# Performance work log

Hardware: AMD Instinct MI355X
Metric: run time of the kernel (lower is better)

Reference implementation:

```python
import jax, jax.numpy as jnp
import numpy as np

EPS = 1e-07


def _windowed_sum(x, window):
    """Zero-padded (TF SAME, stride 1) sliding-window sum along axis 1 via cumsum.
    x: [B, S, C] -> [B, S, C]."""
    pad_left = (window - 1) // 2
    pad_right = (window - 1) - pad_left
    xp = jnp.pad(x, ((0, 0), (pad_left, pad_right), (0, 0)))  # [B, S+W-1, C]
    cs = jnp.cumsum(xp, axis=1)
    cs = jnp.concatenate([jnp.zeros_like(cs[:, :1]), cs], axis=1)  # [B, S+W, C]
    return cs[:, window:] - cs[:, :-window]  # [B, S, C]


def setup_inputs() -> dict:
    key = jax.random.key(0)
    inputs = jax.random.normal(key, (32, 8192, 128), dtype=jnp.float32)
    return {"inputs": inputs, "window_size": 24}


def reference(inputs, window_size):
    W = window_size
    B, S, C = inputs.shape
    # TF AveragePooling1D with SAME padding averages over VALID elements only
    # (padded zeros are excluded from the count).
    ones = jnp.ones((1, S, 1), dtype=inputs.dtype)
    count = _windowed_sum(ones, W)  # [1, S, 1] valid-element counts
    moving_mean = _windowed_sum(inputs, W) / count  # [B, S, C]
    sq = jnp.square(inputs - moving_mean)
    # conv1d with all-ones [W, C, C] kernel, SAME padding: every output channel
    # equals the zero-padded windowed sum of sq summed over ALL input channels.
    sq_tot = jnp.sum(sq, axis=-1, keepdims=True)  # [B, S, 1]
    moving_variance = _windowed_sum(sq_tot, W) / (W - 1)  # [B, S, 1]
    moving_std = jnp.sqrt(moving_variance)  # broadcasts over channels
    return (inputs - moving_mean) / (moving_std + EPS)
```

## Files before the change

kernel.cpp:

```cpp
#include <hip/hip_runtime.h>
#include <math.h>


constexpr int Sdim = 8192;
constexpr int Cdim = 128;
constexpr int TT   = 256;
constexpr int NTb  = Sdim / TT;
constexpr float EPSv = 1e-7f;

typedef unsigned int uintx2 __attribute__((ext_vector_type(2)));

template<bool EDGE>
__device__ __forceinline__ float2 ldg(const float* __restrict__ base, int r) {
    if (EDGE && (unsigned)r >= (unsigned)Sdim) return make_float2(0.f, 0.f);
    return *reinterpret_cast<const float2*>(base + (size_t)r * Cdim);
}

__device__ __forceinline__ void st2(float* p, float a, float b) {
    *reinterpret_cast<float2*>(p) = make_float2(a, b);
}

template<int N>
__device__ __forceinline__ float dpp_ror_add(float v) {
    int r = __builtin_amdgcn_update_dpp(0, __float_as_int(v),
                                        0x120 | N, 0xf, 0xf, true);
    return v + __int_as_float(r);
}

__device__ __forceinline__ float swap32_add(float v) {
    const unsigned u = __float_as_uint(v);
    uintx2 r = __builtin_amdgcn_permlane32_swap(u, u, false, false);
    return __uint_as_float(r.x) + __uint_as_float(r.y);
}

__device__ __forceinline__ float swap16_add(float v) {
    const unsigned u = __float_as_uint(v);
    uintx2 r = __builtin_amdgcn_permlane16_swap(u, u, false, false);
    return __uint_as_float(r.x) + __uint_as_float(r.y);
}

__device__ __forceinline__ float wave_allsum(float v) {
    v = swap32_add(v);
    v = swap16_add(v);
    v = dpp_ror_add<8>(v);
    v = dpp_ror_add<4>(v);
    v = dpp_ror_add<2>(v);
    v = dpp_ror_add<1>(v);
    return v;
}

template<bool EDGE, bool LOAD, int NJ>
__device__ __forceinline__ void chunkN(
    const float* __restrict__ base, float* __restrict__ obase,
    float2 (&Xw)[12], float2 (&Xm)[12], float2 (&Xn)[12],
    float (&Tw)[12], float (&Tr)[12], float2 (&Lb)[12],
    float2& lead, float& varsum, int cb, int t0)
{
    float2 onum[4];
    float  vs4[4];
#pragma unroll
    for (int j = 0; j < NJ; ++j) {
        const int s = cb + j;
        const float2 xold = Xw[j];
        if (LOAD) Xw[j] = ldg<EDGE>(base, s + 24);
        const float2 xmid = Xn[j];
        lead.x += xmid.x - xold.x;
        lead.y += xmid.y - xold.y;
        const float2 xcur = Xm[j];
        float invc;
        if (EDGE) {
            const int cnt = min(s + 12, Sdim - 1) - max(s - 11, 0) + 1;
            invc = __builtin_amdgcn_rcpf((float)cnt);
        } else {
            invc = 1.f / 24.f;
        }
        const float dx = xcur.x - lead.x * invc;
        const float dy = xcur.y - lead.y * invc;
        float st = dx * dx + dy * dy;
        if (EDGE && (unsigned)s >= (unsigned)Sdim) st = 0.f;
        varsum += st - Tr[j];
        Tw[j] = st;
        const float2 wq = Lb[j];
        Lb[j] = lead;
        float invq;
        if (EDGE) {
            const int q = s - 12;
            const int cq = min(q + 12, Sdim - 1) - max(q - 11, 0) + 1;
            invq = __builtin_amdgcn_rcpf((float)cq);
        } else {
            invq = 1.f / 24.f;
        }
        onum[j & 3].x = xold.x - wq.x * invq;
        onum[j & 3].y = xold.y - wq.y * invq;
        vs4[j & 3] = varsum;

        if ((j & 3) == 3) {
            const int q0 = s - 15;
            if (q0 >= t0 && q0 < t0 + TT) {
                const float r0 = wave_allsum(vs4[0]);
                const float r1 = wave_allsum(vs4[1]);
                const float r2 = wave_allsum(vs4[2]);
                const float r3 = wave_allsum(vs4[3]);
                const float i0 = __builtin_amdgcn_rcpf(
                    __builtin_amdgcn_sqrtf(fmaxf(r0, 0.f) * (1.f / 23.f)) + EPSv);
                const float i1 = __builtin_amdgcn_rcpf(
                    __builtin_amdgcn_sqrtf(fmaxf(r1, 0.f) * (1.f / 23.f)) + EPSv);
                const float i2 = __builtin_amdgcn_rcpf(
                    __builtin_amdgcn_sqrtf(fmaxf(r2, 0.f) * (1.f / 23.f)) + EPSv);
                const float i3 = __builtin_amdgcn_rcpf(
                    __builtin_amdgcn_sqrtf(fmaxf(r3, 0.f) * (1.f / 23.f)) + EPSv);
                st2(obase + (size_t)(q0    ) * Cdim, onum[0].x * i0, onum[0].y * i0);
                st2(obase + (size_t)(q0 + 1) * Cdim, onum[1].x * i1, onum[1].y * i1);
                st2(obase + (size_t)(q0 + 2) * Cdim, onum[2].x * i2, onum[2].y * i2);
                st2(obase + (size_t)(q0 + 3) * Cdim, onum[3].x * i3, onum[3].y * i3);
            }
        }
    }
}

template<bool EDGE>
__device__ __forceinline__ void run_tile(
    const float* __restrict__ base, float* __restrict__ obase, int t0)
{
    float2 X0[12], X1[12], X2[12], Lb[12];
    float  T0[12], T1[12], T2[12];
    float2 lead = make_float2(0.f, 0.f);
    float  varsum = 0.f;

#pragma unroll
    for (int j = 0; j < 12; ++j) {
        X0[j] = ldg<EDGE>(base, t0 - 24 + j);
        X1[j] = ldg<EDGE>(base, t0 - 12 + j);
        X2[j] = ldg<EDGE>(base, t0 + j);
        T0[j] = 0.f; T1[j] = 0.f; T2[j] = 0.f;
        Lb[j] = make_float2(0.f, 0.f);
        lead.x += X0[j].x + X1[j].x;
        lead.y += X0[j].y + X1[j].y;
    }

    int cb = t0 - 12;
#pragma unroll 1
    for (int k = 0; k < 7; ++k) {
        chunkN<EDGE, true, 12>(base, obase, X0, X1, X2, T0, T1, Lb, lead, varsum, cb, t0); cb += 12;
        chunkN<EDGE, true, 12>(base, obase, X1, X2, X0, T1, T2, Lb, lead, varsum, cb, t0); cb += 12;
        chunkN<EDGE, true, 12>(base, obase, X2, X0, X1, T2, T0, Lb, lead, varsum, cb, t0); cb += 12;
    }
    chunkN<EDGE, true , 12>(base, obase, X0, X1, X2, T0, T1, Lb, lead, varsum, cb, t0); cb += 12;
    chunkN<EDGE, true , 12>(base, obase, X1, X2, X0, T1, T2, Lb, lead, varsum, cb, t0); cb += 12;
    chunkN<EDGE, false,  4>(base, obase, X2, X0, X1, T2, T0, Lb, lead, varsum, cb, t0);
}

__global__ __launch_bounds__(256, 2)
void mzs_kernel(const float* __restrict__ x, float* __restrict__ y) {
    const int tid  = threadIdx.x;
    const int lane = tid & 63;
    const int wid  = blockIdx.x * 4 + (tid >> 6);
    const int b    = wid >> 5;
    const int ti   = wid & 31;
    const int t0   = ti * TT;
    const float* base  = x + (size_t)b * Sdim * Cdim + lane * 2;
    float*       obase = y + (size_t)b * Sdim * Cdim + lane * 2;
    if (ti == 0 || ti == NTb - 1) run_tile<true >(base, obase, t0);
    else                          run_tile<false>(base, obase, t0);
}

extern "C" void kernel_launch(void* const* d_in, const int* in_sizes, int n_in,
                              void* d_out, int out_size, void* d_ws, size_t ws_size,
                              hipStream_t stream) {
    const float* x = (const float*)d_in[0];
    float* y = (float*)d_out;
    mzs_kernel<<<dim3(256), dim3(256), 0, stream>>>(x, y);
}
```

Measured before the change: 53.56 us.

## Deepen register prefetch ring to four chunks and relax launch bounds

Adds a fourth 12-row register buffer so global loads are issued 36 rows ahead instead of 24, giving more latency hiding per wave. The main loop is restructured into a 12-chunk rotation over four buffers, with loads in the final two chunks gated by a runtime flag. Launch bounds are lowered to one block per SM to allow the larger register footprint. This risks lower occupancy, and the loop now processes 288 rows instead of the previous 268, so it does extra work. The EDGE handling for the extra rows has to be correct.

```diff
diff --git a/kernel.cpp b/kernel.cpp
--- a/kernel.cpp
+++ b/kernel.cpp
@@ -49,20 +49,20 @@
     return v;
 }
 
-template<bool EDGE, bool LOAD, int NJ>
-__device__ __forceinline__ void chunkN(
+template<bool EDGE>
+__device__ __forceinline__ void chunk12(
     const float* __restrict__ base, float* __restrict__ obase,
     float2 (&Xw)[12], float2 (&Xm)[12], float2 (&Xn)[12],
     float (&Tw)[12], float (&Tr)[12], float2 (&Lb)[12],
-    float2& lead, float& varsum, int cb, int t0)
+    float2& lead, float& varsum, int cb, int t0, bool doLoad)
 {
     float2 onum[4];
     float  vs4[4];
 #pragma unroll
-    for (int j = 0; j < NJ; ++j) {
+    for (int j = 0; j < 12; ++j) {
         const int s = cb + j;
         const float2 xold = Xw[j];
-        if (LOAD) Xw[j] = ldg<EDGE>(base, s + 24);
+        if (doLoad) Xw[j] = ldg<EDGE>(base, s + 36);
         const float2 xmid = Xn[j];
         lead.x += xmid.x - xold.x;
         lead.y += xmid.y - xold.y;
@@ -122,7 +122,7 @@
 __device__ __forceinline__ void run_tile(
     const float* __restrict__ base, float* __restrict__ obase, int t0)
 {
-    float2 X0[12], X1[12], X2[12], Lb[12];
+    float2 X0[12], X1[12], X2[12], X3[12], Lb[12];
     float  T0[12], T1[12], T2[12];
     float2 lead = make_float2(0.f, 0.f);
     float  varsum = 0.f;
@@ -132,6 +132,7 @@
         X0[j] = ldg<EDGE>(base, t0 - 24 + j);
         X1[j] = ldg<EDGE>(base, t0 - 12 + j);
         X2[j] = ldg<EDGE>(base, t0 + j);
+        X3[j] = ldg<EDGE>(base, t0 + 12 + j);
         T0[j] = 0.f; T1[j] = 0.f; T2[j] = 0.f;
         Lb[j] = make_float2(0.f, 0.f);
         lead.x += X0[j].x + X1[j].x;
@@ -140,17 +141,24 @@
 
     int cb = t0 - 12;
 #pragma unroll 1
-    for (int k = 0; k < 7; ++k) {
-        chunkN<EDGE, true, 12>(base, obase, X0, X1, X2, T0, T1, Lb, lead, varsum, cb, t0); cb += 12;
-        chunkN<EDGE, true, 12>(base, obase, X1, X2, X0, T1, T2, Lb, lead, varsum, cb, t0); cb += 12;
-        chunkN<EDGE, true, 12>(base, obase, X2, X0, X1, T2, T0, Lb, lead, varsum, cb, t0); cb += 12;
+    for (int r = 0; r < 2; ++r) {
+        const bool lt = (r == 0);
+        chunk12<EDGE>(base, obase, X0, X1, X2, T0, T1, Lb, lead, varsum, cb, t0, true); cb += 12;
+        chunk12<EDGE>(base, obase, X1, X2, X3, T1, T2, Lb, lead, varsum, cb, t0, true); cb += 12;
+        chunk12<EDGE>(base, obase, X2, X3, X0, T2, T0, Lb, lead, varsum, cb, t0, true); cb += 12;
+        chunk12<EDGE>(base, obase, X3, X0, X1, T0, T1, Lb, lead, varsum, cb, t0, true); cb += 12;
+        chunk12<EDGE>(base, obase, X0, X1, X2, T1, T2, Lb, lead, varsum, cb, t0, true); cb += 12;
+        chunk12<EDGE>(base, obase, X1, X2, X3, T2, T0, Lb, lead, varsum, cb, t0, true); cb += 12;
+        chunk12<EDGE>(base, obase, X2, X3, X0, T0, T1, Lb, lead, varsum, cb, t0, true); cb += 12;
+        chunk12<EDGE>(base, obase, X3, X0, X1, T1, T2, Lb, lead, varsum, cb, t0, true); cb += 12;
+        chunk12<EDGE>(base, obase, X0, X1, X2, T2, T0, Lb, lead, varsum, cb, t0, true); cb += 12;
+        chunk12<EDGE>(base, obase, X1, X2, X3, T0, T1, Lb, lead, varsum, cb, t0, true); cb += 12;
+        chunk12<EDGE>(base, obase, X2, X3, X0, T1, T2, Lb, lead, varsum, cb, t0, lt);   cb += 12;
+        chunk12<EDGE>(base, obase, X3, X0, X1, T2, T0, Lb, lead, varsum, cb, t0, lt);   cb += 12;
     }
-    chunkN<EDGE, true , 12>(base, obase, X0, X1, X2, T0, T1, Lb, lead, varsum, cb, t0); cb += 12;
-    chunkN<EDGE, true , 12>(base, obase, X1, X2, X0, T1, T2, Lb, lead, varsum, cb, t0); cb += 12;
-    chunkN<EDGE, false,  4>(base, obase, X2, X0, X1, T2, T0, Lb, lead, varsum, cb, t0);
 }
 
-__global__ __launch_bounds__(256, 2)
+__global__ __launch_bounds__(256, 1)
 void mzs_kernel(const float* __restrict__ x, float* __restrict__ y) {
     const int tid  = threadIdx.x;
     const int lane = tid & 63;
```

After: 53.10 us. Within noise of the previous version (-0.9%).
